# Kernel tuning notes

Measured on AMD Instinct MI355X. Metric: run time of the kernel, lower is better.

The kernel has to match this reference:

```python
import jax, jax.numpy as jnp
import numpy as np

B, L, D = 8, 4096, 512
EPS = 1e-9


def setup_inputs() -> dict:
    key = jax.random.key(0)
    k_h, k_len, k_w1, k_w2 = jax.random.split(key, 4)
    hidden = jax.random.normal(k_h, (B, L, D), dtype=jnp.float32)
    lengths = jax.random.uniform(k_len, (B,), dtype=jnp.float32)  # fraction of valid frames
    W1 = jax.random.normal(k_w1, (D, D), dtype=jnp.float32) * 0.02
    b1 = jnp.zeros((D,), dtype=jnp.float32)
    W2 = jax.random.normal(k_w2, (D, 1), dtype=jnp.float32) * 0.02
    b2 = jnp.zeros((1,), dtype=jnp.float32)
    return {"hidden": hidden, "lengths": lengths, "W1": W1, "b1": b1, "W2": W2, "b2": b2}


def _boundaries(hidden, lengths, W1, b1, W2, b2):
    # Eval mode: dropout is identity, soft_boundaries = sigmoid(logits).
    b, l, d = hidden.shape
    h = jax.nn.gelu(hidden @ W1 + b1, approximate=False)  # torch nn.GELU default = exact erf
    logits = (h @ W2 + b2)[..., 0]                        # [B, L]
    probs = jax.nn.sigmoid(logits)
    soft = probs
    hard = (soft > 0.5).astype(jnp.float32)
    actual_lens = (lengths * l).astype(jnp.int32)         # torch .long() truncation
    pos = jnp.arange(l)[None, :]
    valid = (pos < actual_lens[:, None]).astype(jnp.float32)
    soft = soft * valid
    hard = hard * valid
    masked_probs = probs * valid
    last = jnp.clip(actual_lens - 1, 0, l - 1)
    bidx = jnp.arange(b)
    soft = soft.at[bidx, last].set(1.0)
    hard = hard.at[bidx, last].set(1.0)
    # straight-through estimator: forward == hard, grads flow through soft
    hard_boundaries = hard - jax.lax.stop_gradient(soft) + soft
    return hard_boundaries, masked_probs


def _mean_pool(hard_boundaries, hidden, n_segments):
    # Cumsum-based segment assignment: foo[b,t,s] == 0 iff position t is in segment s.
    hh1 = jnp.cumsum(hard_boundaries, axis=1) - hard_boundaries          # [B, L]
    foo = jnp.arange(n_segments, dtype=hh1.dtype)[None, None, :] - hh1[:, :, None]  # [B, L, S]
    bar = jnp.where(foo == 0, 1.0 - foo, 0.0)                            # matches bar=1-foo; bar[foo!=0]=0
    bar = bar / (bar.sum(axis=1, keepdims=True) + EPS)
    return jnp.einsum('bls,bld->bsd', bar, hidden)


def reference(hidden, lengths, W1, b1, W2, b2):
    hard_boundaries, masked_probs = _boundaries(hidden, lengths, W1, b1, W2, b2)
    num_boundaries_per_sample = jnp.sum(hard_boundaries, axis=1)         # [B]
    # n_segments is a concrete (data-dependent) python int, as in the torch code
    n_segments = int(jnp.max(num_boundaries_per_sample))
    pooled = _mean_pool(hard_boundaries, hidden, n_segments)             # [B, S, D]
    shortened_lengths = num_boundaries_per_sample / max(n_segments, 1)
    return pooled, masked_probs, shortened_lengths, num_boundaries_per_sample
```

## Files before the change

### kernel.cpp

```cpp
#include <hip/hip_runtime.h>
#include <hip/hip_bf16.h>
#include <math.h>

#define BB 8
#define LL 4096
#define DD 512
#define CH 32

typedef __attribute__((ext_vector_type(8))) short bfx8;
typedef __attribute__((ext_vector_type(8))) unsigned short usx8;
typedef __attribute__((ext_vector_type(4))) float fx4;

static __device__ __forceinline__ unsigned short bf_hi(float x) {
    __hip_bfloat16 h = __float2bfloat16(x);
    return *reinterpret_cast<unsigned short*>(&h);
}
static __device__ __forceinline__ float bf_f(unsigned short u) {
    __hip_bfloat16 h = *reinterpret_cast<__hip_bfloat16*>(&u);
    return __bfloat162float(h);
}
static __device__ __forceinline__ void glds16(const void* g, void* l) {
    __builtin_amdgcn_global_load_lds(
        (const __attribute__((address_space(1))) unsigned int*)g,
        (__attribute__((address_space(3))) unsigned int*)l, 16, 0, 0);
}

__global__ __launch_bounds__(256)
void k_split(const float* __restrict__ W1, unsigned short* __restrict__ wt_hi,
             unsigned short* __restrict__ wt_lo) {
    int g = blockIdx.x * 256 + threadIdx.x;
    int n  = g >> 6;
    int kc = g & 63;
    ushort4 h0, h1, l0, l1;
    unsigned short* hp = reinterpret_cast<unsigned short*>(&h0);
    unsigned short* lp = reinterpret_cast<unsigned short*>(&l0);
#pragma unroll
    for (int j = 0; j < 8; j++) {
        float x = W1[(size_t)(kc * 8 + j) * DD + n];
        unsigned short hi = bf_hi(x);
        unsigned short lo = bf_hi(x - bf_f(hi));
        if (j < 4) { hp[j] = hi; lp[j] = lo; }
        else { reinterpret_cast<unsigned short*>(&h1)[j-4] = hi;
               reinterpret_cast<unsigned short*>(&l1)[j-4] = lo; }
    }
    size_t off = (size_t)n * DD + kc * 8;
    *reinterpret_cast<ushort4*>(&wt_hi[off])     = h0;
    *reinterpret_cast<ushort4*>(&wt_hi[off + 4]) = h1;
    *reinterpret_cast<ushort4*>(&wt_lo[off])     = l0;
    *reinterpret_cast<ushort4*>(&wt_lo[off + 4]) = l1;
}

__global__ __launch_bounds__(512, 4)
void k_mfma(const float* __restrict__ hidden,
            const unsigned short* __restrict__ wt_hi,
            const unsigned short* __restrict__ wt_lo,
            const float* __restrict__ b1, const float* __restrict__ W2,
            float* __restrict__ logits) {
    __shared__ __align__(16) char lds[65536];
    const int tid  = threadIdx.x;
    const int wave = tid >> 6;
    const int lane = tid & 63;
    const int grp  = lane >> 4;
    const int lid  = lane & 15;
    const int wr   = wave >> 2;
    const int wc   = wave & 3;

    int wg = (blockIdx.x & 7) * 128 + (blockIdx.x >> 3);
    const int colTile = wg & 3;
    const int rowTile = wg >> 2;
    const int rowBase = rowTile * 128;
    const int colBase = colTile * 128;

    fx4 acc[4][2];
#pragma unroll
    for (int m = 0; m < 4; m++)
#pragma unroll
        for (int n = 0; n < 2; n++) acc[m][n] = {0.f, 0.f, 0.f, 0.f};

    const int arow = tid >> 2;
    const int aq   = tid & 3;
    const float* aSrc = hidden + (size_t)(rowBase + arow) * DD + aq * 16;

    const unsigned short* bsrc[4];
    char* bdst[4];
#pragma unroll
    for (int i = 0; i < 4; i++) {
        int gi = wave * 4 + i;
        int plane = gi >> 4;
        int pi = gi & 15;
        int col = pi * 8 + (lane >> 3);
        int chunk = (lane & 7) ^ (lane >> 3);
        const unsigned short* srcp = plane ? wt_lo : wt_hi;
        bsrc[i] = srcp + (size_t)(colBase + col) * DD + chunk * 8;
        bdst[i] = lds + 32768 + plane * 16384 + pi * 1024;
    }

    float4 av[4];
#pragma unroll
    for (int j = 0; j < 4; j++) av[j] = *reinterpret_cast<const float4*>(aSrc + j * 4);

    for (int kt = 0; kt < 8; kt++) {
        __syncthreads();

#pragma unroll
        for (int j = 0; j < 2; j++) {
            usx8 hi8, lo8;
            float xv[8] = {av[2*j].x, av[2*j].y, av[2*j].z, av[2*j].w,
                           av[2*j+1].x, av[2*j+1].y, av[2*j+1].z, av[2*j+1].w};
#pragma unroll
            for (int e = 0; e < 8; e++) {
                unsigned short h = bf_hi(xv[e]);
                hi8[e] = (short)h;
                lo8[e] = (short)bf_hi(xv[e] - bf_f(h));
            }
            int aoff = arow * 128 + ((aq * 32 + j * 16) ^ ((arow & 7) << 4));
            *reinterpret_cast<usx8*>(lds + aoff)         = hi8;
            *reinterpret_cast<usx8*>(lds + 16384 + aoff) = lo8;
        }
#pragma unroll
        for (int i = 0; i < 4; i++) glds16(bsrc[i] + kt * 64, bdst[i]);

        __syncthreads();

        if (kt < 7) {
#pragma unroll
            for (int j = 0; j < 4; j++)
                av[j] = *reinterpret_cast<const float4*>(aSrc + (kt + 1) * 64 + j * 4);
        }

#pragma unroll
        for (int ks = 0; ks < 2; ks++) {
            const int kb = ks * 64 + grp * 16;
            const int sw = kb ^ ((lid & 7) << 4);
            bfx8 ah[4], bh[2], bl[2], al[4];
#pragma unroll
            for (int m = 0; m < 4; m++) {
                int off = (wr * 64 + m * 16 + lid) * 128 + sw;
                ah[m] = *reinterpret_cast<const bfx8*>(lds + off);
            }
#pragma unroll
            for (int n = 0; n < 2; n++) {
                int off = (wc * 32 + n * 16 + lid) * 128 + sw;
                bh[n] = *reinterpret_cast<const bfx8*>(lds + 32768 + off);
                bl[n] = *reinterpret_cast<const bfx8*>(lds + 49152 + off);
            }
            __builtin_amdgcn_s_setprio(1);
#pragma unroll
            for (int m = 0; m < 4; m++)
#pragma unroll
                for (int n = 0; n < 2; n++)
                    acc[m][n] = __builtin_amdgcn_mfma_f32_16x16x32_bf16(
                        ah[m], bh[n], acc[m][n], 0, 0, 0);
#pragma unroll
            for (int m = 0; m < 4; m++)
#pragma unroll
                for (int n = 0; n < 2; n++)
                    acc[m][n] = __builtin_amdgcn_mfma_f32_16x16x32_bf16(
                        ah[m], bl[n], acc[m][n], 0, 0, 0);
#pragma unroll
            for (int m = 0; m < 4; m++) {
                int off = (wr * 64 + m * 16 + lid) * 128 + sw;
                al[m] = *reinterpret_cast<const bfx8*>(lds + 16384 + off);
            }
#pragma unroll
            for (int m = 0; m < 4; m++)
#pragma unroll
                for (int n = 0; n < 2; n++)
                    acc[m][n] = __builtin_amdgcn_mfma_f32_16x16x32_bf16(
                        al[m], bh[n], acc[m][n], 0, 0, 0);
            __builtin_amdgcn_s_setprio(0);
        }
    }

    float w2v[2], b1v[2];
#pragma unroll
    for (int n = 0; n < 2; n++) {
        int c = colBase + wc * 32 + n * 16 + lid;
        w2v[n] = W2[c]; b1v[n] = b1[c];
    }
    __syncthreads();
    float* parts = reinterpret_cast<float*>(lds);
#pragma unroll
    for (int m = 0; m < 4; m++)
#pragma unroll
        for (int reg = 0; reg < 4; reg++) {
            float p = 0.f;
#pragma unroll
            for (int n = 0; n < 2; n++) {
                float v = acc[m][n][reg] + b1v[n];
                float g = 0.5f * v * (1.0f + erff(v * 0.70710678118654752f));
                p += g * w2v[n];
            }
            p += __shfl_xor(p, 1, 64);
            p += __shfl_xor(p, 2, 64);
            p += __shfl_xor(p, 4, 64);
            p += __shfl_xor(p, 8, 64);
            if (lid == 0)
                parts[(wr * 64 + m * 16 + grp * 4 + reg) * 4 + wc] = p;
        }
    __syncthreads();
    if (tid < 128) {
        float4 v = *reinterpret_cast<const float4*>(parts + tid * 4);
        atomicAdd(&logits[rowBase + tid], v.x + v.y + v.z + v.w);
    }
}

__global__ __launch_bounds__(1024)
void k_bound(const float* __restrict__ logits, const float* __restrict__ lengths,
             const float* __restrict__ b2, float* __restrict__ out, int S,
             int* __restrict__ nseg, int* __restrict__ bpos,
             int* __restrict__ segid) {
    const int b   = blockIdx.x;
    const int tid = threadIdx.x;
    const float alenf = lengths[b] * (float)LL;
    const int alen = (int)alenf;
    const float b2v = b2[0];
    int last = alen - 1;
    if (last < 0) last = 0;
    if (last > LL - 1) last = LL - 1;

    float* out_mp = out + (size_t)BB * S * DD;

    int h[4];
    float4 mp_pack;
    float* mpp = reinterpret_cast<float*>(&mp_pack);
#pragma unroll
    for (int i = 0; i < 4; i++) {
        int t = tid * 4 + i;
        float lg = logits[b * LL + t] + b2v;
        float prob = 1.0f / (1.0f + expf(-lg));
        bool valid = t < alen;
        mpp[i] = valid ? prob : 0.0f;
        int hd = (prob > 0.5f && valid) ? 1 : 0;
        if (t == last) hd = 1;
        h[i] = hd;
    }
    *reinterpret_cast<float4*>(&out_mp[b * LL + tid * 4]) = mp_pack;

    int s4 = h[0] + h[1] + h[2] + h[3];
    const int lane = tid & 63;
    const int wave = tid >> 6;
    int incl = s4;
#pragma unroll
    for (int off = 1; off < 64; off <<= 1) {
        int v = __shfl_up(incl, off, 64);
        if (lane >= off) incl += v;
    }
    __shared__ int wsum[16];
    __shared__ int woff[17];
    if (lane == 63) wsum[wave] = incl;
    __syncthreads();
    if (tid == 0) {
        int r = 0;
        for (int w = 0; w < 16; w++) { woff[w] = r; r += wsum[w]; }
        woff[16] = r;
    }
    __syncthreads();
    int ex = woff[wave] + incl - s4;
    int4 sg_pack;
    int* sgp = reinterpret_cast<int*>(&sg_pack);
#pragma unroll
    for (int i = 0; i < 4; i++) {
        int t = tid * 4 + i;
        sgp[i] = ex;
        if (h[i]) { bpos[b * LL + ex] = t; ex++; }
    }
    *reinterpret_cast<int4*>(&segid[b * LL + tid * 4]) = sg_pack;

    if (tid == 0) {
        int total = woff[16];
        nseg[b] = total;
        float* out_sl = out + (size_t)BB * S * DD + (size_t)BB * LL;
        float* out_nb = out_sl + BB;
        out_nb[b] = (float)total;
        int denom = (S > 1) ? S : 1;
        out_sl[b] = (float)total / (float)denom;
    }
}

__global__ __launch_bounds__(256)
void k_pool2(const float* __restrict__ hidden, const int* __restrict__ nseg,
             const int* __restrict__ bpos, const int* __restrict__ segid,
             float* __restrict__ pooled, int S) {
    const int wave = threadIdx.x >> 6;
    const int lane = threadIdx.x & 63;
    const int g  = blockIdx.x * 4 + wave;
    const int b  = g / (LL / CH);
    const int c  = g % (LL / CH);
    const int t0 = c * CH;
    const int n  = nseg[b];
    const int* sgid = segid + b * LL;
    const int* bp   = bpos + b * LL;
    const float* hb = hidden + (size_t)b * LL * DD;
    float* pb = pooled + (size_t)b * S * DD;

    float4 a0 = {0.f, 0.f, 0.f, 0.f};
    float4 a1 = {0.f, 0.f, 0.f, 0.f};
    int cur = -1;
    int cur_start = 0;

    for (int t = t0; t < t0 + CH; t++) {
        int sg = sgid[t];
        if (sg != cur) {
            if (cur >= 0) {
                int real_end = (cur < n) ? bp[cur] : (LL - 1);
                float inv = 1.0f / (float)(real_end - cur_start + 1);
                float* dst = pb + (size_t)cur * DD;
                bool complete = (cur_start >= t0) && (t - 1 == real_end);
                if (complete) {
                    float4 r0 = {a0.x * inv, a0.y * inv, a0.z * inv, a0.w * inv};
                    float4 r1 = {a1.x * inv, a1.y * inv, a1.z * inv, a1.w * inv};
                    *reinterpret_cast<float4*>(&dst[lane * 4]) = r0;
                    *reinterpret_cast<float4*>(&dst[256 + lane * 4]) = r1;
                } else {
                    atomicAdd(&dst[lane * 4 + 0], a0.x * inv);
                    atomicAdd(&dst[lane * 4 + 1], a0.y * inv);
                    atomicAdd(&dst[lane * 4 + 2], a0.z * inv);
                    atomicAdd(&dst[lane * 4 + 3], a0.w * inv);
                    atomicAdd(&dst[256 + lane * 4 + 0], a1.x * inv);
                    atomicAdd(&dst[256 + lane * 4 + 1], a1.y * inv);
                    atomicAdd(&dst[256 + lane * 4 + 2], a1.z * inv);
                    atomicAdd(&dst[256 + lane * 4 + 3], a1.w * inv);
                }
            }
            if (sg < S) {
                cur = sg;
                cur_start = (sg > 0) ? bp[sg - 1] + 1 : 0;
                a0 = {0.f, 0.f, 0.f, 0.f};
                a1 = {0.f, 0.f, 0.f, 0.f};
            } else {
                cur = -1;
            }
        }
        if (cur >= 0) {
            float4 v0 = *reinterpret_cast<const float4*>(&hb[(size_t)t * DD + lane * 4]);
            float4 v1 = *reinterpret_cast<const float4*>(&hb[(size_t)t * DD + 256 + lane * 4]);
            a0.x += v0.x; a0.y += v0.y; a0.z += v0.z; a0.w += v0.w;
            a1.x += v1.x; a1.y += v1.y; a1.z += v1.z; a1.w += v1.w;
        }
    }
    if (cur >= 0) {
        int real_end = (cur < n) ? bp[cur] : (LL - 1);
        float inv = 1.0f / (float)(real_end - cur_start + 1);
        float* dst = pb + (size_t)cur * DD;
        bool complete = (cur_start >= t0) && (t0 + CH - 1 == real_end);
        if (complete) {
            float4 r0 = {a0.x * inv, a0.y * inv, a0.z * inv, a0.w * inv};
            float4 r1 = {a1.x * inv, a1.y * inv, a1.z * inv, a1.w * inv};
            *reinterpret_cast<float4*>(&dst[lane * 4]) = r0;
            *reinterpret_cast<float4*>(&dst[256 + lane * 4]) = r1;
        } else {
            atomicAdd(&dst[lane * 4 + 0], a0.x * inv);
            atomicAdd(&dst[lane * 4 + 1], a0.y * inv);
            atomicAdd(&dst[lane * 4 + 2], a0.z * inv);
            atomicAdd(&dst[lane * 4 + 3], a0.w * inv);
            atomicAdd(&dst[256 + lane * 4 + 0], a1.x * inv);
            atomicAdd(&dst[256 + lane * 4 + 1], a1.y * inv);
            atomicAdd(&dst[256 + lane * 4 + 2], a1.z * inv);
            atomicAdd(&dst[256 + lane * 4 + 3], a1.w * inv);
        }
    }
}

extern "C" void kernel_launch(void* const* d_in, const int* in_sizes, int n_in,
                              void* d_out, int out_size, void* d_ws, size_t ws_size,
                              hipStream_t stream) {
    const float* hidden  = (const float*)d_in[0];
    const float* lengths = (const float*)d_in[1];
    const float* W1      = (const float*)d_in[2];
    const float* b1      = (const float*)d_in[3];
    const float* W2      = (const float*)d_in[4];
    const float* b2      = (const float*)d_in[5];
    float* out           = (float*)d_out;

    const int S = (out_size - BB * LL - 2 * BB) / (BB * DD);

    float* logits = (float*)d_ws;
    int*   bpos   = (int*)((char*)d_ws + (size_t)BB * LL * 4);
    int*   segid  = (int*)((char*)d_ws + (size_t)2 * BB * LL * 4);
    int*   nseg   = (int*)((char*)d_ws + (size_t)3 * BB * LL * 4);
    unsigned short* wt_hi = (unsigned short*)((char*)d_ws + (size_t)3 * BB * LL * 4 + 1024);
    unsigned short* wt_lo = wt_hi + (size_t)DD * DD;

    hipMemsetAsync(out, 0, (size_t)BB * S * DD * sizeof(float), stream);
    hipMemsetAsync(logits, 0, (size_t)BB * LL * sizeof(float), stream);

    k_split<<<128, 256, 0, stream>>>(W1, wt_hi, wt_lo);
    k_mfma<<<1024, 512, 0, stream>>>(hidden, wt_hi, wt_lo, b1, W2, logits);
    k_bound<<<BB, 1024, 0, stream>>>(logits, lengths, b2, out, S, nseg, bpos, segid);
    k_pool2<<<(BB * (LL / CH)) / 4, 256, 0, stream>>>(hidden, nseg, bpos, segid, out, S);
}
```

Before: 202.5 us.

## Coalesce W1 split via LDS transpose, fold logits zeroing, split pooling by column half

```diff
diff --git a/kernel.cpp b/kernel.cpp
--- a/kernel.cpp
+++ b/kernel.cpp
@@ -5,7 +5,7 @@
 #define BB 8
 #define LL 4096
 #define DD 512
-#define CH 32
+#define CH 16
 
 typedef __attribute__((ext_vector_type(8))) short bfx8;
 typedef __attribute__((ext_vector_type(8))) unsigned short usx8;
@@ -27,27 +27,40 @@
 
 __global__ __launch_bounds__(256)
 void k_split(const float* __restrict__ W1, unsigned short* __restrict__ wt_hi,
-             unsigned short* __restrict__ wt_lo) {
-    int g = blockIdx.x * 256 + threadIdx.x;
-    int n  = g >> 6;
-    int kc = g & 63;
-    ushort4 h0, h1, l0, l1;
-    unsigned short* hp = reinterpret_cast<unsigned short*>(&h0);
-    unsigned short* lp = reinterpret_cast<unsigned short*>(&l0);
-#pragma unroll
-    for (int j = 0; j < 8; j++) {
-        float x = W1[(size_t)(kc * 8 + j) * DD + n];
-        unsigned short hi = bf_hi(x);
-        unsigned short lo = bf_hi(x - bf_f(hi));
-        if (j < 4) { hp[j] = hi; lp[j] = lo; }
-        else { reinterpret_cast<unsigned short*>(&h1)[j-4] = hi;
-               reinterpret_cast<unsigned short*>(&l1)[j-4] = lo; }
-    }
-    size_t off = (size_t)n * DD + kc * 8;
-    *reinterpret_cast<ushort4*>(&wt_hi[off])     = h0;
-    *reinterpret_cast<ushort4*>(&wt_hi[off + 4]) = h1;
-    *reinterpret_cast<ushort4*>(&wt_lo[off])     = l0;
-    *reinterpret_cast<ushort4*>(&wt_lo[off + 4]) = l1;
+             unsigned short* __restrict__ wt_lo, float* __restrict__ logits) {
+    __shared__ float tile[64][65];
+    const int tid = threadIdx.x;
+    const int kt  = blockIdx.x >> 3;
+    const int nt  = blockIdx.x & 7;
+#pragma unroll
+    for (int i = 0; i < 4; i++) {
+        int r  = (tid >> 4) + i * 16;
+        int c4 = tid & 15;
+        float4 v = *reinterpret_cast<const float4*>(
+            &W1[(size_t)(kt * 64 + r) * DD + nt * 64 + c4 * 4]);
+        tile[r][c4 * 4 + 0] = v.x; tile[r][c4 * 4 + 1] = v.y;
+        tile[r][c4 * 4 + 2] = v.z; tile[r][c4 * 4 + 3] = v.w;
+    }
+    int g = blockIdx.x * 256 + tid;
+    logits[g] = 0.f; logits[g + 16384] = 0.f;
+    __syncthreads();
+    const int n  = tid >> 2;
+    const int kq = tid & 3;
+    usx8 h8[2], l8[2];
+#pragma unroll
+    for (int q = 0; q < 2; q++)
+#pragma unroll
+        for (int e = 0; e < 8; e++) {
+            float x = tile[kq * 16 + q * 8 + e][n];
+            unsigned short hi = bf_hi(x);
+            h8[q][e] = (short)hi;
+            l8[q][e] = (short)bf_hi(x - bf_f(hi));
+        }
+    size_t off = (size_t)(nt * 64 + n) * DD + kt * 64 + kq * 16;
+    *reinterpret_cast<usx8*>(&wt_hi[off])     = h8[0];
+    *reinterpret_cast<usx8*>(&wt_hi[off + 8]) = h8[1];
+    *reinterpret_cast<usx8*>(&wt_lo[off])     = l8[0];
+    *reinterpret_cast<usx8*>(&wt_lo[off + 8]) = l8[1];
 }
 
 __global__ __launch_bounds__(512, 4)
@@ -101,7 +114,6 @@
 
     for (int kt = 0; kt < 8; kt++) {
         __syncthreads();
-
 #pragma unroll
         for (int j = 0; j < 2; j++) {
             usx8 hi8, lo8;
@@ -221,14 +233,15 @@
 
     float* out_mp = out + (size_t)BB * S * DD;
 
+    float4 lg4 = *reinterpret_cast<const float4*>(&logits[b * LL + tid * 4]);
+    const float* lgp = reinterpret_cast<const float*>(&lg4);
     int h[4];
     float4 mp_pack;
     float* mpp = reinterpret_cast<float*>(&mp_pack);
 #pragma unroll
     for (int i = 0; i < 4; i++) {
         int t = tid * 4 + i;
-        float lg = logits[b * LL + t] + b2v;
-        float prob = 1.0f / (1.0f + expf(-lg));
+        float prob = 1.0f / (1.0f + expf(-(lgp[i] + b2v)));
         bool valid = t < alen;
         mpp[i] = valid ? prob : 0.0f;
         int hd = (prob > 0.5f && valid) ? 1 : 0;
@@ -285,21 +298,28 @@
     const int wave = threadIdx.x >> 6;
     const int lane = threadIdx.x & 63;
     const int g  = blockIdx.x * 4 + wave;
-    const int b  = g / (LL / CH);
-    const int c  = g % (LL / CH);
+    const int hf = g & 1;
+    const int cg = g >> 1;
+    const int b  = cg / (LL / CH);
+    const int c  = cg % (LL / CH);
     const int t0 = c * CH;
+    const int col = hf * 256 + lane * 4;
     const int n  = nseg[b];
     const int* sgid = segid + b * LL;
     const int* bp   = bpos + b * LL;
-    const float* hb = hidden + (size_t)b * LL * DD;
-    float* pb = pooled + (size_t)b * S * DD;
-
-    float4 a0 = {0.f, 0.f, 0.f, 0.f};
-    float4 a1 = {0.f, 0.f, 0.f, 0.f};
+    const float* hb = hidden + (size_t)b * LL * DD + col;
+    float* pb = pooled + (size_t)b * S * DD + col;
+
+    float4 a = {0.f, 0.f, 0.f, 0.f};
     int cur = -1;
     int cur_start = 0;
 
+    float4 vnext = *reinterpret_cast<const float4*>(&hb[(size_t)t0 * DD]);
+#pragma unroll
     for (int t = t0; t < t0 + CH; t++) {
+        float4 v = vnext;
+        if (t + 1 < t0 + CH)
+            vnext = *reinterpret_cast<const float4*>(&hb[(size_t)(t + 1) * DD]);
         int sg = sgid[t];
         if (sg != cur) {
             if (cur >= 0) {
@@ -308,36 +328,24 @@
                 float* dst = pb + (size_t)cur * DD;
                 bool complete = (cur_start >= t0) && (t - 1 == real_end);
                 if (complete) {
-                    float4 r0 = {a0.x * inv, a0.y * inv, a0.z * inv, a0.w * inv};
-                    float4 r1 = {a1.x * inv, a1.y * inv, a1.z * inv, a1.w * inv};
-                    *reinterpret_cast<float4*>(&dst[lane * 4]) = r0;
-                    *reinterpret_cast<float4*>(&dst[256 + lane * 4]) = r1;
+                    float4 r = {a.x * inv, a.y * inv, a.z * inv, a.w * inv};
+                    *reinterpret_cast<float4*>(dst) = r;
                 } else {
-                    atomicAdd(&dst[lane * 4 + 0], a0.x * inv);
-                    atomicAdd(&dst[lane * 4 + 1], a0.y * inv);
-                    atomicAdd(&dst[lane * 4 + 2], a0.z * inv);
-                    atomicAdd(&dst[lane * 4 + 3], a0.w * inv);
-                    atomicAdd(&dst[256 + lane * 4 + 0], a1.x * inv);
-                    atomicAdd(&dst[256 + lane * 4 + 1], a1.y * inv);
-                    atomicAdd(&dst[256 + lane * 4 + 2], a1.z * inv);
-                    atomicAdd(&dst[256 + lane * 4 + 3], a1.w * inv);
+                    atomicAdd(dst + 0, a.x * inv);
+                    atomicAdd(dst + 1, a.y * inv);
+                    atomicAdd(dst + 2, a.z * inv);
+                    atomicAdd(dst + 3, a.w * inv);
                 }
             }
             if (sg < S) {
                 cur = sg;
                 cur_start = (sg > 0) ? bp[sg - 1] + 1 : 0;
-                a0 = {0.f, 0.f, 0.f, 0.f};
-                a1 = {0.f, 0.f, 0.f, 0.f};
+                a = {0.f, 0.f, 0.f, 0.f};
             } else {
                 cur = -1;
             }
         }
-        if (cur >= 0) {
-            float4 v0 = *reinterpret_cast<const float4*>(&hb[(size_t)t * DD + lane * 4]);
-            float4 v1 = *reinterpret_cast<const float4*>(&hb[(size_t)t * DD + 256 + lane * 4]);
-            a0.x += v0.x; a0.y += v0.y; a0.z += v0.z; a0.w += v0.w;
-            a1.x += v1.x; a1.y += v1.y; a1.z += v1.z; a1.w += v1.w;
-        }
+        if (cur >= 0) { a.x += v.x; a.y += v.y; a.z += v.z; a.w += v.w; }
     }
     if (cur >= 0) {
         int real_end = (cur < n) ? bp[cur] : (LL - 1);
@@ -345,19 +353,13 @@
         float* dst = pb + (size_t)cur * DD;
         bool complete = (cur_start >= t0) && (t0 + CH - 1 == real_end);
         if (complete) {
-            float4 r0 = {a0.x * inv, a0.y * inv, a0.z * inv, a0.w * inv};
-            float4 r1 = {a1.x * inv, a1.y * inv, a1.z * inv, a1.w * inv};
-            *reinterpret_cast<float4*>(&dst[lane * 4]) = r0;
-            *reinterpret_cast<float4*>(&dst[256 + lane * 4]) = r1;
+            float4 r = {a.x * inv, a.y * inv, a.z * inv, a.w * inv};
+            *reinterpret_cast<float4*>(dst) = r;
         } else {
-            atomicAdd(&dst[lane * 4 + 0], a0.x * inv);
-            atomicAdd(&dst[lane * 4 + 1], a0.y * inv);
-            atomicAdd(&dst[lane * 4 + 2], a0.z * inv);
-            atomicAdd(&dst[lane * 4 + 3], a0.w * inv);
-            atomicAdd(&dst[256 + lane * 4 + 0], a1.x * inv);
-            atomicAdd(&dst[256 + lane * 4 + 1], a1.y * inv);
-            atomicAdd(&dst[256 + lane * 4 + 2], a1.z * inv);
-            atomicAdd(&dst[256 + lane * 4 + 3], a1.w * inv);
+            atomicAdd(dst + 0, a.x * inv);
+            atomicAdd(dst + 1, a.y * inv);
+            atomicAdd(dst + 2, a.z * inv);
+            atomicAdd(dst + 3, a.w * inv);
         }
     }
 }
@@ -383,10 +385,9 @@
     unsigned short* wt_lo = wt_hi + (size_t)DD * DD;
 
     hipMemsetAsync(out, 0, (size_t)BB * S * DD * sizeof(float), stream);
-    hipMemsetAsync(logits, 0, (size_t)BB * LL * sizeof(float), stream);
-
-    k_split<<<128, 256, 0, stream>>>(W1, wt_hi, wt_lo);
+
+    k_split<<<64, 256, 0, stream>>>(W1, wt_hi, wt_lo, logits);
     k_mfma<<<1024, 512, 0, stream>>>(hidden, wt_hi, wt_lo, b1, W2, logits);
     k_bound<<<BB, 1024, 0, stream>>>(logits, lengths, b2, out, S, nseg, bpos, segid);
-    k_pool2<<<(BB * (LL / CH)) / 4, 256, 0, stream>>>(hidden, nseg, bpos, segid, out, S);
-}
+    k_pool2<<<(BB * (LL / CH) * 2) / 4, 256, 0, stream>>>(hidden, nseg, bpos, segid, out, S);
+}
```

Result: slower. 207.3 us (+2.4%).
